# Kernel tuning notes

Measured on AMD Instinct MI355X. Metric: run time of the kernel, lower is better.

Reference implementation:

```python
import jax, jax.numpy as jnp
import numpy as np

D_MODEL = 1024
N_HEADS = 16
D_HEAD = D_MODEL // N_HEADS
RANK = 16
DECAY = 0.95
ALPHA_MAX = 0.05
BETA = 0.01


def setup_inputs() -> dict:
    key = jax.random.key(0)
    ks = jax.random.split(key, 9)
    B, T = 4, 2048
    s = 0.02  # init scale for weights
    return {
        "hidden_states": jax.random.normal(ks[0], (B, T, D_MODEL), jnp.float32),
        "m_gate": jax.random.uniform(ks[1], (B, T), jnp.float32),
        "alpha_scale": jax.random.uniform(ks[2], (B, T, N_HEADS), jnp.float32),
        "Wq": jax.random.normal(ks[3], (D_MODEL, D_MODEL), jnp.float32) * s,
        "Wk": jax.random.normal(ks[4], (D_MODEL, D_MODEL), jnp.float32) * s,
        "Wv": jax.random.normal(ks[5], (D_MODEL, D_MODEL), jnp.float32) * s,
        "Wo": jax.random.normal(ks[6], (D_MODEL, D_MODEL), jnp.float32) * s,
        "Wa": jax.random.normal(ks[7], (N_HEADS, D_MODEL), jnp.float32) * s,
        "ba": jnp.zeros((N_HEADS,), jnp.float32),
        "mix_logit": jnp.zeros((N_HEADS,), jnp.float32),
    }


def reference(hidden_states, m_gate, alpha_scale, Wq, Wk, Wv, Wo, Wa, ba, mix_logit):
    B, T, D = hidden_states.shape
    H, Dh, R = N_HEADS, D_HEAD, RANK
    # batched projections (Linear: x @ W.T), then split heads
    q = (hidden_states @ Wq.T).reshape(B, T, H, Dh)
    k = (hidden_states @ Wk.T).reshape(B, T, H, Dh)
    v = (hidden_states @ Wv.T).reshape(B, T, H, Dh)
    # alpha computed under torch.no_grad in the original -> stop_gradient
    alpha = jax.nn.sigmoid(hidden_states @ Wa.T + ba)  # [B,T,H]
    alpha = alpha * m_gate[..., None] * alpha_scale
    alpha = jnp.minimum(alpha, ALPHA_MAX)
    alpha = jax.lax.stop_gradient(alpha)

    inv_sqrt_dh = 1.0 / (Dh ** 0.5)

    def step(carry, xs):
        U, V = carry  # U: [B,H,Dh,R], V: [B,H,R,Dh]
        q_t, k_t, v_t, a_t = xs  # [B,H,Dh], [B,H,Dh], [B,H,Dh], [B,H]
        U = DECAY * U
        V = DECAY * V
        ku = jnp.einsum('bhd,bhdr->bhr', k_t, U)
        a = a_t[..., None, None]
        U = U + a * jnp.einsum('bhd,bhr->bhdr', k_t, ku)
        V = V + a * jnp.einsum('bhr,bhd->bhrd', ku, v_t)
        U = U - BETA * jnp.clip(U, -1.0, 1.0)
        V = V - BETA * jnp.clip(V, -1.0, 1.0)
        # whole fast-weight update is no_grad in the original
        U = jax.lax.stop_gradient(U)
        V = jax.lax.stop_gradient(V)
        q_norm = q_t * inv_sqrt_dh
        k_fast = jnp.einsum('bhdr,bhrd->bhd', U, V)  # [B,H,Dh]
        score_slow = jnp.sum(q_norm * k_t, axis=-1)  # [B,H]
        score_fast = jnp.sum(q_norm * k_fast, axis=-1)
        logits = jnp.stack([score_slow, score_fast], axis=-1) + mix_logit[None, :, None]
        mix = jax.nn.softmax(logits, axis=-1)  # [B,H,2]
        y = mix[..., 0:1] * v_t + mix[..., 1:2] * k_fast  # [B,H,Dh]
        return (U, V), y

    U0 = jnp.zeros((B, H, Dh, R), hidden_states.dtype)
    V0 = jnp.zeros((B, H, R, Dh), hidden_states.dtype)
    xs = (jnp.moveaxis(q, 1, 0), jnp.moveaxis(k, 1, 0),
          jnp.moveaxis(v, 1, 0), jnp.moveaxis(alpha, 1, 0))
    _, ys = jax.lax.scan(step, (U0, V0), xs)  # ys: [T,B,H,Dh]
    y = jnp.moveaxis(ys, 0, 1).reshape(B, T, D)
    return y @ Wo.T
```

## Files before the change

kernel.cpp:

```cpp
#include <hip/hip_runtime.h>
#include <hip/hip_bf16.h>
#include <stdint.h>

#define D_MODEL 1024
#define N_HEADS 16
#define D_HEAD  64
#define SEQ_T   2048
#define BATCH   4

typedef unsigned short u16;
typedef __bf16 bf16x8 __attribute__((ext_vector_type(8)));
typedef float  f32x4  __attribute__((ext_vector_type(4)));

#define QNT 32

__device__ __forceinline__ u16 f2bf(float x) {
  unsigned u = __float_as_uint(x);
  u += 0x7fffu + ((u >> 16) & 1u);
  return (u16)(u >> 16);
}
__device__ __forceinline__ unsigned pk2(float a, float b) {
  return (unsigned)f2bf(a) | ((unsigned)f2bf(b) << 16);
}
__device__ __forceinline__ void cp16(const u16* g, u16* l) {
  __builtin_amdgcn_global_load_lds(
      (const __attribute__((address_space(1))) unsigned int*)g,
      (__attribute__((address_space(3))) unsigned int*)l, 16, 0, 0);
}

__global__ __launch_bounds__(256) void cast_kernel(const float* __restrict__ hs,
                                                   const float* __restrict__ wq,
                                                   const float* __restrict__ wk,
                                                   const float* __restrict__ wv,
                                                   const float* __restrict__ wo,
                                                   u16* __restrict__ Xb,
                                                   u16* __restrict__ Wb) {
  int g = blockIdx.x * 256 + threadIdx.x;
  const float4* src; uint4* dst;
  if (g < (1 << 20)) {
    src = (const float4*)hs + 2 * (size_t)g;
    dst = (uint4*)Xb + g;
  } else {
    int j = g - (1 << 20);
    int R = j >> 7;
    int col8 = j & 127;
    const float* s;
    int srow;
    if (R < 2048) {
      int h = R >> 7, c = R & 127, jj = c >> 4, l = c & 15;
      srow = h * 64 + (jj >> 1) * 16 + l;
      s = (jj & 1) ? wk : wq;
    } else if (R < 3072) { s = wv; srow = R - 2048; }
    else                 { s = wo; srow = R - 3072; }
    src = (const float4*)s + (size_t)srow * 256 + col8 * 2;
    dst = (uint4*)Wb + (size_t)R * 128 + col8;
  }
  float4 lo = src[0], hi = src[1];
  uint4 o;
  o.x = pk2(lo.x, lo.y); o.y = pk2(lo.z, lo.w);
  o.z = pk2(hi.x, hi.y); o.w = pk2(hi.z, hi.w);
  *dst = o;
}

#define QVM(n) asm volatile("s_waitcnt vmcnt(" #n ")" ::: "memory")

__global__ __launch_bounds__(256, 2) void gemm_qkv_kernel(const u16* __restrict__ A,
                                                          const u16* __restrict__ B,
                                                          u16* __restrict__ Vb,
                                                          float* __restrict__ S) {
  __shared__ u16 Ls[36864];
  const int tid  = threadIdx.x;
  const int w    = tid >> 6;
  const int l    = tid & 63;
  const int quad = l >> 4;
  const int l16  = l & 15;
  const int wm   = (w >> 1) * 128;
  const int wn   = (w & 1) * 64;

  const int id  = blockIdx.y * 24 + blockIdx.x;
  const int id2 = (id & 7) * 96 + (id >> 3);
  const int bm  = id2 / 24;
  const int bn  = id2 % 24;

  const int srow = w * 16 + (l >> 2);
  const int schk = (l & 3) * 8;
  const u16* aS[4]; const u16* bS[2];
  #pragma unroll
  for (int r = 0; r < 4; ++r)
    aS[r] = A + (size_t)(bm * 256 + r * 64 + srow) * 1024 + schk;
  #pragma unroll
  for (int r = 0; r < 2; ++r)
    bS[r] = B + (size_t)(bn * 128 + r * 64 + srow) * 1024 + schk;
  u16* dA = Ls + w * 512 + l * 8;
  u16* dB = Ls + 24576 + w * 512 + l * 8;

  f32x4 acc[8][4];
  #pragma unroll
  for (int i = 0; i < 8; ++i)
    #pragma unroll
    for (int j = 0; j < 4; ++j) acc[i][j] = (f32x4){0.f, 0.f, 0.f, 0.f};

  #pragma unroll
  for (int r = 0; r < 4; ++r) cp16(aS[r] + 0 * 32, dA + 0 * 8192 + r * 2048);
  #pragma unroll
  for (int r = 0; r < 2; ++r) cp16(bS[r] + 0 * 32, dB + 0 * 4096 + r * 2048);
  #pragma unroll
  for (int r = 0; r < 4; ++r) cp16(aS[r] + 1 * 32, dA + 1 * 8192 + r * 2048);
  #pragma unroll
  for (int r = 0; r < 2; ++r) cp16(bS[r] + 1 * 32, dB + 1 * 4096 + r * 2048);
  QVM(6);
  __builtin_amdgcn_s_barrier();

  int rbuf = 0, sbuf = 2;
  #pragma unroll 1
  for (int t = 0; t < QNT; ++t) {
    if (t + 2 < QNT) {
      #pragma unroll
      for (int r = 0; r < 4; ++r)
        cp16(aS[r] + (t + 2) * 32, dA + sbuf * 8192 + r * 2048);
      #pragma unroll
      for (int r = 0; r < 2; ++r)
        cp16(bS[r] + (t + 2) * 32, dB + sbuf * 4096 + r * 2048);
    }
    const u16* Ar = Ls + rbuf * 8192;
    const u16* Br = Ls + 24576 + rbuf * 4096;
    bf16x8 af[8], bfr[4];
    #pragma unroll
    for (int i = 0; i < 8; ++i)
      af[i] = *(const bf16x8*)(Ar + (wm + i * 16 + l16) * 32 + quad * 8);
    #pragma unroll
    for (int j = 0; j < 4; ++j)
      bfr[j] = *(const bf16x8*)(Br + (wn + j * 16 + l16) * 32 + quad * 8);
    __builtin_amdgcn_s_setprio(1);
    #pragma unroll
    for (int i = 0; i < 8; ++i)
      #pragma unroll
      for (int j = 0; j < 4; ++j)
        acc[i][j] = __builtin_amdgcn_mfma_f32_16x16x32_bf16(af[i], bfr[j], acc[i][j], 0, 0, 0);
    __builtin_amdgcn_s_setprio(0);
    if (t + 2 < QNT) { QVM(6); } else { QVM(0); }
    __builtin_amdgcn_s_barrier();
    rbuf = (rbuf == 2) ? 0 : rbuf + 1;
    sbuf = (sbuf == 2) ? 0 : sbuf + 1;
  }

  if (bn < 16) {
    float part[8][4];
    #pragma unroll
    for (int i = 0; i < 8; ++i)
      #pragma unroll
      for (int e = 0; e < 4; ++e)
        part[i][e] = acc[i][0][e] * acc[i][1][e] + acc[i][2][e] * acc[i][3][e];
    #pragma unroll
    for (int m = 1; m <= 8; m <<= 1)
      #pragma unroll
      for (int i = 0; i < 8; ++i)
        #pragma unroll
        for (int e = 0; e < 4; ++e)
          part[i][e] += __shfl_xor(part[i][e], m);
    float* Sp = (float*)Ls;
    if (l16 == 0) {
      #pragma unroll
      for (int i = 0; i < 8; ++i)
        #pragma unroll
        for (int e = 0; e < 4; ++e)
          Sp[(wm + i * 16 + quad * 4 + e) * 2 + (w & 1)] = part[i][e];
    }
    __syncthreads();
    {
      int row = tid;
      float s = (Sp[row * 2] + Sp[row * 2 + 1]) * 0.125f;
      S[(size_t)(bm * 256 + row) * N_HEADS + bn] = 1.f / (1.f + __expf(-s));
    }
  } else {
    const int cb = (bn - 16) * 128;
    #pragma unroll
    for (int i = 0; i < 8; ++i)
      #pragma unroll
      for (int j = 0; j < 4; ++j)
        #pragma unroll
        for (int e = 0; e < 4; ++e) {
          int row = bm * 256 + wm + i * 16 + quad * 4 + e;
          int col = cb + wn + j * 16 + l16;
          Vb[(size_t)row * D_MODEL + col] = f2bf(acc[i][j][e]);
        }
  }
}

__global__ __launch_bounds__(256, 2) void gemm_out_kernel(const u16* __restrict__ A,
                                                          const u16* __restrict__ B,
                                                          const float* __restrict__ S,
                                                          float* __restrict__ C) {
  constexpr int N = D_MODEL;
  __shared__ u16 Ls[32768];
  const int tid  = threadIdx.x;
  const int l    = tid & 63;
  const int w    = tid >> 6;
  const int quad = l >> 4;
  const int l16  = l & 15;
  const int wm   = (w >> 1) * 64;
  const int wn   = (w & 1) * 64;

  const int id  = blockIdx.y * 8 + blockIdx.x;
  const int id2 = (id & 7) * 64 + (id >> 3);
  const int bm  = (id2 >> 3) * 128;
  const int bn  = (id2 & 7) * 128;

  const int srow = tid >> 3;
  const int sch  = ((tid & 7) ^ (srow & 7)) * 8;
  const u16* aG[4]; const u16* bG[4];
  #pragma unroll
  for (int u = 0; u < 4; ++u) {
    aG[u] = A + (size_t)(bm + u * 32 + srow) * 1024 + sch;
    bG[u] = B + (size_t)(bn + u * 32 + srow) * 1024 + sch;
  }
  u16* dA = Ls + tid * 8;
  u16* dB = Ls + 16384 + tid * 8;

#define OSTAGE(t, b)                                                           \
  do {                                                                         \
    _Pragma("unroll") for (int _u = 0; _u < 4; ++_u) {                         \
      cp16(aG[_u] + (t) * 64, dA + (b) * 8192 + _u * 2048);                    \
      cp16(bG[_u] + (t) * 64, dB + (b) * 8192 + _u * 2048);                    \
    }                                                                          \
  } while (0)

  const int rc0 = ((0 + quad) ^ (l16 & 7)) * 8;
  const int rc1 = ((4 + quad) ^ (l16 & 7)) * 8;

  const float* Srow[4];
  #pragma unroll
  for (int i = 0; i < 4; ++i)
    Srow[i] = S + (size_t)(bm + wm + i * 16 + quad * 4) * N_HEADS;

  f32x4 acc[4][4];
  #pragma unroll
  for (int i = 0; i < 4; ++i)
    #pragma unroll
    for (int j = 0; j < 4; ++j) acc[i][j] = (f32x4){0.f, 0.f, 0.f, 0.f};
  const f32x4 z4 = (f32x4){0.f, 0.f, 0.f, 0.f};

  OSTAGE(0, 0);
  QVM(0);
  __builtin_amdgcn_s_barrier();

  #pragma unroll 1
  for (int t = 0; t < 16; ++t) {
    float sv[4][4];
    #pragma unroll
    for (int i = 0; i < 4; ++i)
      #pragma unroll
      for (int e = 0; e < 4; ++e)
        sv[i][e] = Srow[i][e * N_HEADS + t];
    if (t + 1 < 16) OSTAGE(t + 1, (t + 1) & 1);
    const u16* Ar = Ls + (t & 1) * 8192;
    const u16* Br = Ls + 16384 + (t & 1) * 8192;
    bf16x8 af[2][4], bfr[2][4];
    #pragma unroll
    for (int i = 0; i < 4; ++i) {
      af[0][i]  = *(const bf16x8*)(Ar + (wm + i * 16 + l16) * 64 + rc0);
      af[1][i]  = *(const bf16x8*)(Ar + (wm + i * 16 + l16) * 64 + rc1);
      bfr[0][i] = *(const bf16x8*)(Br + (wn + i * 16 + l16) * 64 + rc0);
      bfr[1][i] = *(const bf16x8*)(Br + (wn + i * 16 + l16) * 64 + rc1);
    }
    __builtin_amdgcn_s_setprio(1);
    #pragma unroll
    for (int jh = 0; jh < 2; ++jh) {
      f32x4 pacc[4][2];
      #pragma unroll
      for (int i = 0; i < 4; ++i)
        #pragma unroll
        for (int jj = 0; jj < 2; ++jj)
          pacc[i][jj] = __builtin_amdgcn_mfma_f32_16x16x32_bf16(
              af[0][i], bfr[0][jh * 2 + jj], z4, 0, 0, 0);
      #pragma unroll
      for (int i = 0; i < 4; ++i)
        #pragma unroll
        for (int jj = 0; jj < 2; ++jj)
          pacc[i][jj] = __builtin_amdgcn_mfma_f32_16x16x32_bf16(
              af[1][i], bfr[1][jh * 2 + jj], pacc[i][jj], 0, 0, 0);
      #pragma unroll
      for (int i = 0; i < 4; ++i)
        #pragma unroll
        for (int jj = 0; jj < 2; ++jj)
          #pragma unroll
          for (int e = 0; e < 4; ++e)
            acc[i][jh * 2 + jj][e] += sv[i][e] * pacc[i][jj][e];
    }
    __builtin_amdgcn_s_setprio(0);
    QVM(0);
    __builtin_amdgcn_s_barrier();
  }

  #pragma unroll
  for (int i = 0; i < 4; ++i)
    #pragma unroll
    for (int j = 0; j < 4; ++j)
      #pragma unroll
      for (int e = 0; e < 4; ++e) {
        int row = bm + wm + i * 16 + quad * 4 + e;
        int col = bn + wn + j * 16 + l16;
        C[(size_t)row * N + col] = acc[i][j][e];
      }
}

extern "C" void kernel_launch(void* const* d_in, const int* in_sizes, int n_in,
                              void* d_out, int out_size, void* d_ws, size_t ws_size,
                              hipStream_t stream) {
  const float* hs = (const float*)d_in[0];
  const float* Wq = (const float*)d_in[3];
  const float* Wk = (const float*)d_in[4];
  const float* Wv = (const float*)d_in[5];
  const float* Wo = (const float*)d_in[6];

  char* ws = (char*)d_ws;
  u16*  Xb = (u16*)ws;
  u16*  Wb = (u16*)(ws + (16u << 20));
  u16*  Vb = (u16*)(ws + (24u << 20));
  float* Sb = (float*)(ws + (40u << 20));
  float* out = (float*)d_out;

  cast_kernel<<<6144, 256, 0, stream>>>(hs, Wq, Wk, Wv, Wo, Xb, Wb);
  gemm_qkv_kernel<<<dim3(24, 32), 256, 0, stream>>>(Xb, Wb, Vb, Sb);
  gemm_out_kernel<<<dim3(8, 64), 256, 0, stream>>>(
      Vb, Wb + (size_t)3072 * D_MODEL, Sb, out);
}
```

Measured before the change: 186.6 us.

## Fuse hidden-state fp32-to-bf16 cast into QKV GEMM A-tile loading

```diff
diff --git a/kernel.cpp b/kernel.cpp
--- a/kernel.cpp
+++ b/kernel.cpp
@@ -22,39 +22,35 @@
 __device__ __forceinline__ unsigned pk2(float a, float b) {
   return (unsigned)f2bf(a) | ((unsigned)f2bf(b) << 16);
 }
+__device__ __forceinline__ unsigned cvtpk(float lo, float hi) {
+  unsigned r;
+  asm("v_cvt_pk_bf16_f32 %0, %1, %2" : "=v"(r) : "v"(lo), "v"(hi));
+  return r;
+}
 __device__ __forceinline__ void cp16(const u16* g, u16* l) {
   __builtin_amdgcn_global_load_lds(
       (const __attribute__((address_space(1))) unsigned int*)g,
       (__attribute__((address_space(3))) unsigned int*)l, 16, 0, 0);
 }
 
-__global__ __launch_bounds__(256) void cast_kernel(const float* __restrict__ hs,
-                                                   const float* __restrict__ wq,
+__global__ __launch_bounds__(256) void cast_kernel(const float* __restrict__ wq,
                                                    const float* __restrict__ wk,
                                                    const float* __restrict__ wv,
                                                    const float* __restrict__ wo,
-                                                   u16* __restrict__ Xb,
                                                    u16* __restrict__ Wb) {
-  int g = blockIdx.x * 256 + threadIdx.x;
-  const float4* src; uint4* dst;
-  if (g < (1 << 20)) {
-    src = (const float4*)hs + 2 * (size_t)g;
-    dst = (uint4*)Xb + g;
-  } else {
-    int j = g - (1 << 20);
-    int R = j >> 7;
-    int col8 = j & 127;
-    const float* s;
-    int srow;
-    if (R < 2048) {
-      int h = R >> 7, c = R & 127, jj = c >> 4, l = c & 15;
-      srow = h * 64 + (jj >> 1) * 16 + l;
-      s = (jj & 1) ? wk : wq;
-    } else if (R < 3072) { s = wv; srow = R - 2048; }
-    else                 { s = wo; srow = R - 3072; }
-    src = (const float4*)s + (size_t)srow * 256 + col8 * 2;
-    dst = (uint4*)Wb + (size_t)R * 128 + col8;
-  }
+  int j = blockIdx.x * 256 + threadIdx.x;
+  int R = j >> 7;
+  int col8 = j & 127;
+  const float* s;
+  int srow;
+  if (R < 2048) {
+    int h = R >> 7, c = R & 127, jj = c >> 4, l = c & 15;
+    srow = h * 64 + (jj >> 1) * 16 + l;
+    s = (jj & 1) ? wk : wq;
+  } else if (R < 3072) { s = wv; srow = R - 2048; }
+  else                 { s = wo; srow = R - 3072; }
+  const float4* src = (const float4*)s + (size_t)srow * 256 + col8 * 2;
+  uint4* dst = (uint4*)Wb + (size_t)R * 128 + col8;
   float4 lo = src[0], hi = src[1];
   uint4 o;
   o.x = pk2(lo.x, lo.y); o.y = pk2(lo.z, lo.w);
@@ -64,7 +60,7 @@
 
 #define QVM(n) asm volatile("s_waitcnt vmcnt(" #n ")" ::: "memory")
 
-__global__ __launch_bounds__(256, 2) void gemm_qkv_kernel(const u16* __restrict__ A,
+__global__ __launch_bounds__(256, 2) void gemm_qkv_kernel(const float* __restrict__ A32,
                                                           const u16* __restrict__ B,
                                                           u16* __restrict__ Vb,
                                                           float* __restrict__ S) {
@@ -82,66 +78,96 @@
   const int bm  = id2 / 24;
   const int bn  = id2 % 24;
 
+  const int c4 = tid & 3;
+  const int r0 = tid >> 2;
+  const float* aG[4];
+  #pragma unroll
+  for (int u = 0; u < 4; ++u)
+    aG[u] = A32 + (size_t)(bm * 256 + u * 64 + r0) * 1024 + c4 * 8;
+  u16* aW = Ls + r0 * 32 + c4 * 8;
+
   const int srow = w * 16 + (l >> 2);
   const int schk = (l & 3) * 8;
-  const u16* aS[4]; const u16* bS[2];
-  #pragma unroll
-  for (int r = 0; r < 4; ++r)
-    aS[r] = A + (size_t)(bm * 256 + r * 64 + srow) * 1024 + schk;
+  const u16* bS[2];
   #pragma unroll
   for (int r = 0; r < 2; ++r)
     bS[r] = B + (size_t)(bn * 128 + r * 64 + srow) * 1024 + schk;
-  u16* dA = Ls + w * 512 + l * 8;
   u16* dB = Ls + 24576 + w * 512 + l * 8;
 
+  float4 av0[4][2], av1[4][2];
+
+#define QAL(t, AV)                                                             \
+  do {                                                                         \
+    _Pragma("unroll") for (int _u = 0; _u < 4; ++_u) {                         \
+      AV[_u][0] = *(const float4*)(aG[_u] + (t) * 32);                         \
+      AV[_u][1] = *(const float4*)(aG[_u] + (t) * 32 + 4);                     \
+    }                                                                          \
+  } while (0)
+#define QAW(AV, slot)                                                          \
+  do {                                                                         \
+    _Pragma("unroll") for (int _u = 0; _u < 4; ++_u) {                         \
+      uint4 _o;                                                                \
+      _o.x = cvtpk(AV[_u][0].x, AV[_u][0].y);                                  \
+      _o.y = cvtpk(AV[_u][0].z, AV[_u][0].w);                                  \
+      _o.z = cvtpk(AV[_u][1].x, AV[_u][1].y);                                  \
+      _o.w = cvtpk(AV[_u][1].z, AV[_u][1].w);                                  \
+      *(uint4*)(aW + (slot) * 8192 + _u * 2048) = _o;                          \
+    }                                                                          \
+  } while (0)
+#define QSB(t, slot)                                                           \
+  do {                                                                         \
+    cp16(bS[0] + (t) * 32, dB + (slot) * 4096);                                \
+    cp16(bS[1] + (t) * 32, dB + (slot) * 4096 + 2048);                         \
+  } while (0)
+
   f32x4 acc[8][4];
   #pragma unroll
   for (int i = 0; i < 8; ++i)
     #pragma unroll
     for (int j = 0; j < 4; ++j) acc[i][j] = (f32x4){0.f, 0.f, 0.f, 0.f};
 
-  #pragma unroll
-  for (int r = 0; r < 4; ++r) cp16(aS[r] + 0 * 32, dA + 0 * 8192 + r * 2048);
-  #pragma unroll
-  for (int r = 0; r < 2; ++r) cp16(bS[r] + 0 * 32, dB + 0 * 4096 + r * 2048);
-  #pragma unroll
-  for (int r = 0; r < 4; ++r) cp16(aS[r] + 1 * 32, dA + 1 * 8192 + r * 2048);
-  #pragma unroll
-  for (int r = 0; r < 2; ++r) cp16(bS[r] + 1 * 32, dB + 1 * 4096 + r * 2048);
-  QVM(6);
+  QAL(0, av0);
+  QSB(0, 0);
+  QAW(av0, 0);
+  QAL(1, av1);
+  QSB(1, 1);
+  QVM(10);
   __builtin_amdgcn_s_barrier();
 
-  int rbuf = 0, sbuf = 2;
+  int rbuf = 0, wbuf = 1, sbuf = 2;
+#define QBODY(t, AVL, AVW)                                                     \
+  do {                                                                         \
+    if ((t) + 2 < QNT) {                                                       \
+      QAL((t) + 2, AVL);                                  \
+      QSB((t) + 2, sbuf);                                          \
+    }                                                                          \
+    if ((t) + 1 < QNT) QAW(AVW, wbuf);   \
+    const u16* Ar = Ls + rbuf * 8192;                                          \
+    const u16* Br = Ls + 24576 + rbuf * 4096;                                  \
+    bf16x8 af[8], bfr[4];                                                      \
+    _Pragma("unroll") for (int _i = 0; _i < 8; ++_i)                           \
+      af[_i] = *(const bf16x8*)(Ar + (wm + _i * 16 + l16) * 32 + quad * 8);    \
+    _Pragma("unroll") for (int _j = 0; _j < 4; ++_j)                           \
+      bfr[_j] = *(const bf16x8*)(Br + (wn + _j * 16 + l16) * 32 + quad * 8);   \
+    __builtin_amdgcn_s_setprio(1);                                             \
+    _Pragma("unroll") for (int _i = 0; _i < 8; ++_i)                           \
+      _Pragma("unroll") for (int _j = 0; _j < 4; ++_j)                         \
+        acc[_i][_j] = __builtin_amdgcn_mfma_f32_16x16x32_bf16(                 \
+            af[_i], bfr[_j], acc[_i][_j], 0, 0, 0);                            \
+    __builtin_amdgcn_s_setprio(0);                                             \
+    if ((t) + 2 < QNT) { QVM(10); }                                            \
+    else if ((t) == QNT - 2) { QVM(0); }                                       \
+    __builtin_amdgcn_s_barrier();                                              \
+    rbuf = rbuf == 2 ? 0 : rbuf + 1;                                           \
+    wbuf = wbuf == 2 ? 0 : wbuf + 1;                                           \
+    sbuf = sbuf == 2 ? 0 : sbuf + 1;                                           \
+  } while (0)
+
   #pragma unroll 1
-  for (int t = 0; t < QNT; ++t) {
-    if (t + 2 < QNT) {
-      #pragma unroll
-      for (int r = 0; r < 4; ++r)
-        cp16(aS[r] + (t + 2) * 32, dA + sbuf * 8192 + r * 2048);
-      #pragma unroll
-      for (int r = 0; r < 2; ++r)
-        cp16(bS[r] + (t + 2) * 32, dB + sbuf * 4096 + r * 2048);
-    }
-    const u16* Ar = Ls + rbuf * 8192;
-    const u16* Br = Ls + 24576 + rbuf * 4096;
-    bf16x8 af[8], bfr[4];
-    #pragma unroll
-    for (int i = 0; i < 8; ++i)
-      af[i] = *(const bf16x8*)(Ar + (wm + i * 16 + l16) * 32 + quad * 8);
-    #pragma unroll
-    for (int j = 0; j < 4; ++j)
-      bfr[j] = *(const bf16x8*)(Br + (wn + j * 16 + l16) * 32 + quad * 8);
-    __builtin_amdgcn_s_setprio(1);
-    #pragma unroll
-    for (int i = 0; i < 8; ++i)
-      #pragma unroll
-      for (int j = 0; j < 4; ++j)
-        acc[i][j] = __builtin_amdgcn_mfma_f32_16x16x32_bf16(af[i], bfr[j], acc[i][j], 0, 0, 0);
-    __builtin_amdgcn_s_setprio(0);
-    if (t + 2 < QNT) { QVM(6); } else { QVM(0); }
-    __builtin_amdgcn_s_barrier();
-    rbuf = (rbuf == 2) ? 0 : rbuf + 1;
-    sbuf = (sbuf == 2) ? 0 : sbuf + 1;
+  for (int tp = 0; tp < QNT / 2; ++tp) {
+    const int t0 = 2 * tp;
+    QBODY(t0, av0, av1);
+    QBODY(t0 + 1, av1, av0);
   }
 
   if (bn < 16) {
@@ -314,14 +340,13 @@
   const float* Wo = (const float*)d_in[6];
 
   char* ws = (char*)d_ws;
-  u16*  Xb = (u16*)ws;
-  u16*  Wb = (u16*)(ws + (16u << 20));
-  u16*  Vb = (u16*)(ws + (24u << 20));
-  float* Sb = (float*)(ws + (40u << 20));
+  u16*  Wb = (u16*)ws;
+  u16*  Vb = (u16*)(ws + (8u << 20));
+  float* Sb = (float*)(ws + (24u << 20));
   float* out = (float*)d_out;
 
-  cast_kernel<<<6144, 256, 0, stream>>>(hs, Wq, Wk, Wv, Wo, Xb, Wb);
-  gemm_qkv_kernel<<<dim3(24, 32), 256, 0, stream>>>(Xb, Wb, Vb, Sb);
+  cast_kernel<<<2048, 256, 0, stream>>>(Wq, Wk, Wv, Wo, Wb);
+  gemm_qkv_kernel<<<dim3(24, 32), 256, 0, stream>>>(hs, Wb, Vb, Sb);
   gemm_out_kernel<<<dim3(8, 64), 256, 0, stream>>>(
       Vb, Wb + (size_t)3072 * D_MODEL, Sb, out);
 }
```

New measurement: 275.1 us. 1.47x slower.
